# Kernel optimization log

Measured on AMD Instinct MI355X. Metric: run time of the kernel, lower is better.

Reference implementation:

```python
import jax, jax.numpy as jnp
import numpy as np

N = 100_000      # nodes
E = 1_600_000    # edges (before self-loops)
F_IN = 128       # num_features
H = 128          # nhid
G = 512          # graphs in batch
C = 10           # num_classes
EPS = 1e-5       # BatchNorm eps


def setup_inputs() -> dict:
    key = jax.random.key(0)
    ks = jax.random.split(key, 24)
    x = jax.random.normal(ks[0], (N, F_IN), jnp.float32)
    edge_index = jax.random.randint(ks[1], (2, E), 0, N, dtype=jnp.int64)
    batch = jnp.sort(jax.random.randint(ks[2], (N,), 0, G, dtype=jnp.int64))

    def lin(k, fi, fo):
        return jax.random.normal(k, (fi, fo), jnp.float32) / np.sqrt(fi).astype(np.float32)

    inp = dict(x=x, edge_index=edge_index, batch=batch)
    inp.update(
        W1=lin(ks[3], F_IN, H), b1=jnp.zeros((H,), jnp.float32),
        g1=jnp.ones((H,), jnp.float32), be1=jnp.zeros((H,), jnp.float32),
        W2=lin(ks[4], H, H), b2=jnp.zeros((H,), jnp.float32),
        g2=jnp.ones((H,), jnp.float32), be2=jnp.zeros((H,), jnp.float32),
        W3=lin(ks[5], H, H), b3=jnp.zeros((H,), jnp.float32),
        g3=jnp.ones((H,), jnp.float32), be3=jnp.zeros((H,), jnp.float32),
        gp=jnp.ones((H,), jnp.float32), bep=jnp.zeros((H,), jnp.float32),
        lw1=lin(ks[6], H, H), lb1=jnp.zeros((H,), jnp.float32),
        lw2=lin(ks[7], H, C), lb2=jnp.zeros((C,), jnp.float32),
    )
    return inp


def _batchnorm(h, g, b):
    # training-mode BatchNorm1d: batch stats, biased variance
    m = h.mean(axis=0)
    v = h.var(axis=0)
    return g * (h - m) * jax.lax.rsqrt(v + EPS) + b


def _gcn(h, W, b, src, dst, norm, n):
    # GCNConv: h @ W, then normalized gather-scatter aggregation
    h = h @ W
    msg = h[src] * norm[:, None]                     # [E+N, H] gather
    out = jax.ops.segment_sum(msg, dst, num_segments=n)
    return out + b


def reference(x, edge_index, batch, W1, b1, g1, be1, W2, b2, g2, be2,
              W3, b3, g3, be3, gp, bep, lw1, lb1, lw2, lb2):
    n = x.shape[0]
    loops = jnp.arange(n, dtype=edge_index.dtype)
    src = jnp.concatenate([edge_index[0], loops])
    dst = jnp.concatenate([edge_index[1], loops])
    # symmetric normalization D^{-1/2} (A+I) D^{-1/2}
    deg = jax.ops.segment_sum(jnp.ones_like(src, dtype=x.dtype), dst, num_segments=n)
    dis = jnp.where(deg > 0, jax.lax.rsqrt(jnp.maximum(deg, 1.0)), 0.0)
    norm = dis[src] * dis[dst]

    h = jax.nn.relu(_batchnorm(_gcn(x, W1, b1, src, dst, norm, n), g1, be1))
    h = jax.nn.relu(_batchnorm(_gcn(h, W2, b2, src, dst, norm, n), g2, be2))
    h = jax.nn.relu(_batchnorm(_gcn(h, W3, b3, src, dst, norm, n), g3, be3))

    # global_mean_pool over graph ids
    counts = jax.ops.segment_sum(jnp.ones((n,), x.dtype), batch, num_segments=G)
    pooled = jax.ops.segment_sum(h, batch, num_segments=G) / jnp.maximum(counts, 1.0)[:, None]

    z = _batchnorm(pooled, gp, bep)
    z = jax.nn.relu(z @ lw1 + lb1)
    # dropout_ratio=0.0 -> identity
    z = z @ lw2 + lb2
    return jax.nn.log_softmax(z, axis=-1)
```

## Files before the change

### kernel.cpp

```cpp
#include <hip/hip_runtime.h>
#include <hip/hip_bf16.h>
#include <cstdint>

#define HDIM 128

typedef __bf16 bf16x8 __attribute__((ext_vector_type(8)));
typedef unsigned short usx8 __attribute__((ext_vector_type(8)));
typedef float fx4 __attribute__((ext_vector_type(4)));

__device__ __forceinline__ float bf2f(unsigned short u) {
    unsigned int x = ((unsigned int)u) << 16;
    return __uint_as_float(x);
}
__device__ __forceinline__ unsigned short f2bf(float f) {
    unsigned int x = __float_as_uint(f);
    x += 0x7fffu + ((x >> 16) & 1u);
    return (unsigned short)(x >> 16);
}

__device__ __forceinline__ void detect_local(const unsigned int* xw, const unsigned int* eiw,
                                             int& f0, int& f1) {
    int sane = 0;
    for (int k = 0; k < 64; k++) {
        unsigned int w = xw[k];
        unsigned short ss[2] = {(unsigned short)(w & 0xffffu), (unsigned short)(w >> 16)};
        for (int q = 0; q < 2; q++) {
            int e = (ss[q] >> 7) & 0xFF;
            if ((ss[q] & 0x7fffu) == 0 || (e >= 100 && e <= 140)) sane++;
        }
    }
    f0 = (sane >= 110) ? 1 : 0;
    int zeros = 0;
    for (int k = 1; k < 64; k += 2)
        if (eiw[k] == 0) zeros++;
    f1 = (zeros >= 24) ? 1 : 0;
}

struct ParamTab {
    const void* p[15];
    int n[15];
    int off[15];
};

__global__ void phase1(const unsigned int* __restrict__ xw, const unsigned int* __restrict__ eiw,
                       const void* __restrict__ ei, const void* __restrict__ batch,
                       const void* __restrict__ W1, const void* __restrict__ W2,
                       const void* __restrict__ W3, ParamTab tab, int* __restrict__ flags,
                       float* __restrict__ gsumAll, int* __restrict__ Ct,
                       unsigned short* __restrict__ wconv, unsigned short* __restrict__ Wf,
                       int* __restrict__ goff, int* __restrict__ gcnt, int E, int N, int G,
                       int NB, int ntiles, int TILE) {
    __shared__ int h[1024];
    __shared__ int lf0s, lf1s;
    int b = blockIdx.x, t = threadIdx.x;
    if (t == 0) {
        int a0, a1;
        detect_local(xw, eiw, a0, a1);
        lf0s = a0;
        lf1s = a1;
    }
    __syncthreads();
    int lf0 = lf0s, lf1 = lf1s;
    if (b < ntiles) {
        for (int i = t; i < NB; i += 256) h[i] = 0;
        __syncthreads();
        int base = b * TILE;
        for (int i = t; i < TILE; i += 256) {
            int idx = base + i;
            if (idx < E) {
                int d = lf1 ? (int)((const long long*)ei)[(size_t)E + idx]
                            : ((const int*)ei)[(size_t)E + idx];
                atomicAdd(&h[d >> 9], 1);
            }
        }
        __syncthreads();
        for (int k = t; k < NB; k += 256) Ct[k * ntiles + b] = h[k];
    } else if (b < ntiles + 15) {
        int pb = b - ntiles;
        const void* src = tab.p[pb];
        int n = tab.n[pb];
        unsigned short* o = wconv + tab.off[pb];
        if (lf0) {
            const unsigned short* s = (const unsigned short*)src;
            for (int i = t; i < n; i += 256) o[i] = s[i];
        } else {
            const float* s = (const float*)src;
            for (int i = t; i < n; i += 256) o[i] = f2bf(s[i]);
        }
    } else if (b < ntiles + 17) {
        int gi = (b - ntiles - 15) * 256 + t;
        if (gi < G) {
            auto getb = [&](int i) -> int {
                return lf1 ? (int)((const long long*)batch)[i] : ((const int*)batch)[i];
            };
            auto lower = [&](int val) -> int {
                int lo = 0, hi = N;
                while (lo < hi) {
                    int mid = (lo + hi) >> 1;
                    if (getb(mid) < val) lo = mid + 1;
                    else hi = mid;
                }
                return lo;
            };
            int lo = lower(gi), hi = lower(gi + 1);
            goff[gi] = lo;
            gcnt[gi] = hi - lo;
        }
    } else if (b < ntiles + 17 + 24) {
        int idx = (b - ntiles - 17) * 256 + t;
        int layer = idx >> 11;
        int rem = idx & 2047;
        int kt = rem >> 9;
        int nt = (rem >> 6) & 7;
        int lane = rem & 63;
        const void* W = (layer == 0) ? W1 : ((layer == 1) ? W2 : W3);
        int row = lane & 15, quad = lane >> 4;
        unsigned short* o = Wf + ((size_t)layer * 2048 + (size_t)((kt * 8 + nt) * 64 + lane)) * 8;
#pragma unroll
        for (int j = 0; j < 8; j++) {
            int k = kt * 32 + quad * 8 + j;
            int off = k * HDIM + nt * 16 + row;
            o[j] = lf0 ? ((const unsigned short*)W)[off] : f2bf(((const float*)W)[off]);
        }
    } else {
        for (int i = t; i < 12288; i += 256) gsumAll[i] = 0.f;
        if (t == 0) {
            flags[0] = lf0;
            flags[1] = lf1;
        }
    }
}

__global__ void s1_scan(int* __restrict__ Ct, int* __restrict__ btot, int NB, int ntiles) {
    __shared__ int buf[512];
    int b = blockIdx.x, t = threadIdx.x;
    int v = (t < ntiles) ? Ct[b * ntiles + t] : 0;
    buf[t] = v;
    __syncthreads();
    for (int o = 1; o < 512; o <<= 1) {
        int a = (t >= o) ? buf[t - o] : 0;
        __syncthreads();
        buf[t] += a;
        __syncthreads();
    }
    if (t < ntiles) Ct[b * ntiles + t] = buf[t] - v;
    if (t == 0) btot[b] = buf[511];
}

__global__ void p1_scatter(const void* __restrict__ ei, const int* __restrict__ flags,
                           const int* __restrict__ Ct, const int* __restrict__ btot,
                           unsigned int* __restrict__ pairs, int E, int NB, int ntiles,
                           int TILE) {
    __shared__ int cur[1024];
    __shared__ int bb[256];
    int tile = blockIdx.x, t = threadIdx.x;
    int v = (t < NB) ? btot[t] : 0;
    bb[t] = v;
    __syncthreads();
    for (int o = 1; o < 256; o <<= 1) {
        int a = (t >= o) ? bb[t - o] : 0;
        __syncthreads();
        bb[t] += a;
        __syncthreads();
    }
    if (t < NB) cur[t] = (bb[t] - v) + Ct[t * ntiles + tile];
    __syncthreads();
    int base = tile * TILE;
    bool i64 = flags[1] != 0;
    for (int i = t; i < TILE; i += 256) {
        int idx = base + i;
        if (idx < E) {
            int s, d;
            if (i64) {
                s = (int)((const long long*)ei)[idx];
                d = (int)((const long long*)ei)[(size_t)E + idx];
            } else {
                s = ((const int*)ei)[idx];
                d = ((const int*)ei)[(size_t)E + idx];
            }
            int pos = atomicAdd(&cur[d >> 9], 1);
            pairs[pos] = ((unsigned)(d & 511) << 23) | (unsigned)s;
        }
    }
}

__global__ void p2_build(const unsigned int* __restrict__ pairs, const int* __restrict__ btot,
                         int* __restrict__ csrc, int* __restrict__ offs, int* __restrict__ cnt,
                         float* __restrict__ dis, int E, int N, int NB) {
    __shared__ int hist[512];
    __shared__ int start[512];
    __shared__ int cur[512];
    __shared__ int ps[256];
    __shared__ int bb[256];
    __shared__ int sh_excl[256];
    int b = blockIdx.x, t = threadIdx.x;
    int node0 = b * 512;
    int v = (t < NB) ? btot[t] : 0;
    bb[t] = v;
    __syncthreads();
    for (int o = 1; o < 256; o <<= 1) {
        int a = (t >= o) ? bb[t - o] : 0;
        __syncthreads();
        bb[t] += a;
        __syncthreads();
    }
    sh_excl[t] = bb[t] - v;
    for (int i = t; i < 512; i += 256) hist[i] = 0;
    __syncthreads();
    int lo = sh_excl[b];
    int hi = lo + ((b < NB) ? btot[b] : 0);
    for (int i = lo + t; i < hi; i += 256) {
        atomicAdd(&hist[pairs[i] >> 23], 1);
    }
    __syncthreads();
    ps[t] = hist[2 * t] + hist[2 * t + 1];
    __syncthreads();
    for (int o = 1; o < 256; o <<= 1) {
        int a = (t >= o) ? ps[t - o] : 0;
        __syncthreads();
        ps[t] += a;
        __syncthreads();
    }
    int e = t ? ps[t - 1] : 0;
    start[2 * t] = e;
    start[2 * t + 1] = e + hist[2 * t];
    __syncthreads();
    for (int i = t; i < 512; i += 256) {
        cur[i] = 0;
        int node = node0 + i;
        if (node < N) {
            offs[node] = lo + start[i];
            cnt[node] = hist[i];
            dis[node] = rsqrtf((float)(hist[i] + 1));
        }
    }
    __syncthreads();
    for (int i = lo + t; i < hi; i += 256) {
        unsigned int p = pairs[i];
        int l = p >> 23;
        int pos = lo + start[l] + atomicAdd(&cur[l], 1);
        csrc[pos] = (int)(p & 0x7fffffu);
    }
}

__global__ __launch_bounds__(256) void mm_mfma(const void* __restrict__ A,
                                               const unsigned short* __restrict__ Wf,
                                               unsigned short* __restrict__ C, int M,
                                               const float* __restrict__ gsumPrev,
                                               const unsigned short* __restrict__ gamma,
                                               const unsigned short* __restrict__ beta,
                                               const float* __restrict__ dis,
                                               const int* __restrict__ flags, int l0mode,
                                               float invn) {
    __shared__ float scs[128], shs[128];
    __shared__ unsigned short ldsC[4 * 16 * 136];
    int t = threadIdx.x;
    if (!l0mode && t < 128) {
        float s = 0.f, s2 = 0.f;
#pragma unroll
        for (int r = 0; r < 16; r++) {
            s += gsumPrev[r * 256 + t];
            s2 += gsumPrev[r * 256 + 128 + t];
        }
        float m = s * invn;
        float vv = s2 * invn - m * m;
        float sc = bf2f(gamma[t]) * rsqrtf(vv + 1e-5f);
        scs[t] = sc;
        shs[t] = bf2f(beta[t]) - m * sc;
    }
    __syncthreads();
    int gid = blockIdx.x * blockDim.x + t;
    int wave = gid >> 6;
    int lane = t & 63;
    int wv = t >> 6;
    int m0 = wave * 16;
    if (m0 >= M) return;
    int row = lane & 15, quad = lane >> 4;
    bool xfp32 = l0mode && !flags[0];
    const unsigned short* arow = (const unsigned short*)A + (size_t)(m0 + row) * HDIM + quad * 8;
    const float* arowf = (const float*)A + (size_t)(m0 + row) * HDIM + quad * 8;
    const unsigned short* ablk = (const unsigned short*)A;
    fx4 acc[8];
#pragma unroll
    for (int k = 0; k < 8; k++) acc[k] = (fx4){0.f, 0.f, 0.f, 0.f};
#pragma unroll
    for (int kt = 0; kt < 4; kt++) {
        bf16x8 a;
        if (xfp32) {
            fx4 f0 = *(const fx4*)(arowf + kt * 32);
            fx4 f1 = *(const fx4*)(arowf + kt * 32 + 4);
            usx8 tt;
#pragma unroll
            for (int q = 0; q < 4; q++) tt[q] = f2bf(f0[q]);
#pragma unroll
            for (int q = 0; q < 4; q++) tt[4 + q] = f2bf(f1[q]);
            a = __builtin_bit_cast(bf16x8, tt);
        } else if (l0mode) {
            usx8 raw = *(const usx8*)(arow + kt * 32);
            a = __builtin_bit_cast(bf16x8, raw);
        } else {
            int c0 = kt * 32 + quad * 8;
            usx8 raw =
                *(const usx8*)(ablk + ((size_t)(c0 >> 4) * M + (m0 + row)) * 16 + (c0 & 15));
            fx4 s0 = *(const fx4*)&scs[c0];
            fx4 s1 = *(const fx4*)&scs[c0 + 4];
            fx4 h0 = *(const fx4*)&shs[c0];
            fx4 h1 = *(const fx4*)&shs[c0 + 4];
            usx8 tt;
#pragma unroll
            for (int q = 0; q < 4; q++)
                tt[q] = f2bf(fmaxf(s0[q] * bf2f(raw[q]) + h0[q], 0.f));
#pragma unroll
            for (int q = 0; q < 4; q++)
                tt[4 + q] = f2bf(fmaxf(s1[q] * bf2f(raw[4 + q]) + h1[q], 0.f));
            a = __builtin_bit_cast(bf16x8, tt);
        }
        const unsigned short* wf = Wf + ((size_t)(kt * 8) * 64 + lane) * 8;
#pragma unroll
        for (int nt = 0; nt < 8; nt++) {
            bf16x8 bfr = __builtin_bit_cast(bf16x8, *(const usx8*)(wf + (size_t)nt * 64 * 8));
            acc[nt] = __builtin_amdgcn_mfma_f32_16x16x32_bf16(a, bfr, acc[nt], 0, 0, 0);
        }
    }
    float dsc[4];
#pragma unroll
    for (int r = 0; r < 4; r++) dsc[r] = dis[m0 + quad * 4 + r];
    unsigned short* lw = ldsC + wv * 16 * 136;
#pragma unroll
    for (int nt = 0; nt < 8; nt++) {
        int col = nt * 16 + row;
#pragma unroll
        for (int r = 0; r < 4; r++) {
            lw[(quad * 4 + r) * 136 + col] = f2bf(acc[nt][r] * dsc[r]);
        }
    }
    int sub8 = lane & 7, cbw = lane >> 3;
#pragma unroll
    for (int k = 0; k < 4; k++) {
        int ci = k * 8 + sub8;
        int nd = ci >> 1, half = ci & 1;
        if (m0 + nd < M) {
            const unsigned short* src = lw + nd * 136 + cbw * 16 + half * 8;
            unsigned short* dst = C + ((size_t)cbw * M + (m0 + nd)) * 16 + half * 8;
            *(usx8*)dst = *(const usx8*)src;
        }
    }
}

__global__ void aggregate(const unsigned short* __restrict__ hw, const float* __restrict__ dis,
                          const int* __restrict__ offs, const int* __restrict__ cnt,
                          const int* __restrict__ csrc, const unsigned short* __restrict__ bias,
                          unsigned short* __restrict__ agg, float* __restrict__ gsum16, int n) {
    __shared__ float red[256 * 8];
    int t = threadIdx.x;
    int lane = t & 63;
    int wv = t >> 6;
    int cb = blockIdx.x & 7;
    int gidx = blockIdx.x >> 3;
    int P = gridDim.x >> 3;
    int colOff = (lane & 1) * 8;
    usx8 bv = *(const usx8*)(bias + cb * 16 + colOff);
    const unsigned short* hslice = hw + (size_t)cb * n * 16;
    unsigned short* aslice = agg + (size_t)cb * n * 16;
    float csum[8], csq[8];
#pragma unroll
    for (int q = 0; q < 8; q++) {
        csum[q] = 0.f;
        csq[q] = 0.f;
    }
    for (int node0 = gidx * 128; node0 < n; node0 += P * 128) {
        int node = node0 + wv * 32 + (lane >> 1);
        if (node < n) {
            usx8 sv = *(const usx8*)(hslice + (size_t)node * 16 + colOff);
            float a[8];
#pragma unroll
            for (int q = 0; q < 8; q++) a[q] = bf2f(sv[q]);
            int o = offs[node], c = cnt[node];
            int s0 = (c > 0) ? csrc[o] : 0;
            int s1 = (c > 1) ? csrc[o + 1] : 0;
            int s2 = (c > 2) ? csrc[o + 2] : 0;
            int s3 = (c > 3) ? csrc[o + 3] : 0;
            int j = 0;
            while (j < c) {
                usx8 v0 = *(const usx8*)(hslice + (size_t)s0 * 16 + colOff);
                usx8 v1 = *(const usx8*)(hslice + (size_t)s1 * 16 + colOff);
                usx8 v2 = *(const usx8*)(hslice + (size_t)s2 * 16 + colOff);
                usx8 v3 = *(const usx8*)(hslice + (size_t)s3 * 16 + colOff);
                s0 = (j + 4 < c) ? csrc[o + j + 4] : 0;
                s1 = (j + 5 < c) ? csrc[o + j + 5] : 0;
                s2 = (j + 6 < c) ? csrc[o + j + 6] : 0;
                s3 = (j + 7 < c) ? csrc[o + j + 7] : 0;
#pragma unroll
                for (int q = 0; q < 8; q++) a[q] += bf2f(v0[q]);
                if (j + 1 < c) {
#pragma unroll
                    for (int q = 0; q < 8; q++) a[q] += bf2f(v1[q]);
                }
                if (j + 2 < c) {
#pragma unroll
                    for (int q = 0; q < 8; q++) a[q] += bf2f(v2[q]);
                }
                if (j + 3 < c) {
#pragma unroll
                    for (int q = 0; q < 8; q++) a[q] += bf2f(v3[q]);
                }
                j += 4;
            }
            float di = dis[node];
            usx8 ov;
#pragma unroll
            for (int q = 0; q < 8; q++) {
                float val = bf2f(bv[q]) + di * a[q];
                ov[q] = f2bf(val);
                float vr = bf2f(ov[q]);
                csum[q] += vr;
                csq[q] += vr * vr;
            }
            __builtin_nontemporal_store(ov, (usx8*)(aslice + (size_t)node * 16 + colOff));
        }
    }
    int rep = (gidx & 15) * 256;
#pragma unroll
    for (int q = 0; q < 8; q++) red[t * 8 + q] = csum[q];
    __syncthreads();
    for (int s = 128; s >= 2; s >>= 1) {
        if (t < s) {
#pragma unroll
            for (int q = 0; q < 8; q++) red[t * 8 + q] += red[(t + s) * 8 + q];
        }
        __syncthreads();
    }
    if (t < 2) {
#pragma unroll
        for (int q = 0; q < 8; q++)
            atomicAdd(&gsum16[rep + cb * 16 + t * 8 + q], red[t * 8 + q]);
    }
    __syncthreads();
#pragma unroll
    for (int q = 0; q < 8; q++) red[t * 8 + q] = csq[q];
    __syncthreads();
    for (int s = 128; s >= 2; s >>= 1) {
        if (t < s) {
#pragma unroll
            for (int q = 0; q < 8; q++) red[t * 8 + q] += red[(t + s) * 8 + q];
        }
        __syncthreads();
    }
    if (t < 2) {
#pragma unroll
        for (int q = 0; q < 8; q++)
            atomicAdd(&gsum16[rep + 128 + cb * 16 + t * 8 + q], red[t * 8 + q]);
    }
}

__global__ void pool(const unsigned short* __restrict__ hin, const int* __restrict__ goff,
                     const int* __restrict__ gcnt, const float* __restrict__ gsum3,
                     const unsigned short* __restrict__ gamma,
                     const unsigned short* __restrict__ beta, float* __restrict__ pooled,
                     float invn, int N_) {
    __shared__ float scs[128], shs[128];
    __shared__ float ls[256];
    int g = blockIdx.x, t = threadIdx.x;
    if (t < 128) {
        float s = 0.f, s2 = 0.f;
#pragma unroll
        for (int r = 0; r < 16; r++) {
            s += gsum3[r * 256 + t];
            s2 += gsum3[r * 256 + 128 + t];
        }
        float m = s * invn;
        float vv = s2 * invn - m * m;
        float sc = bf2f(gamma[t]) * rsqrtf(vv + 1e-5f);
        scs[t] = sc;
        shs[t] = bf2f(beta[t]) - m * sc;
    }
    __syncthreads();
    int c = t & 127, p = t >> 7;
    float scale = scs[c], shift = shs[c];
    int s = goff[g], cn = gcnt[g];
    const unsigned short* base = hin + (size_t)(c >> 4) * N_ * 16 + (c & 15);
    float acc = 0.f;
    for (int r = s + p; r < s + cn; r += 2)
        acc += fmaxf(scale * bf2f(base[(size_t)r * 16]) + shift, 0.f);
    ls[t] = acc;
    __syncthreads();
    if (t < 128) pooled[(size_t)g * HDIM + t] = (ls[t] + ls[t + 128]) / fmaxf((float)cn, 1.f);
}
__global__ void pooled_bn(const float* __restrict__ pooled, const unsigned short* __restrict__ g,
                          const unsigned short* __restrict__ be, float* __restrict__ psc,
                          float* __restrict__ psh, int G_) {
    int t = threadIdx.x;
    int c = t & 127, p = t >> 7;
    float s = 0.f, s2 = 0.f;
    for (int r = p; r < G_; r += 4) {
        float v = pooled[(size_t)r * HDIM + c];
        s += v;
        s2 += v * v;
    }
    __shared__ float ls[512], ls2[512];
    ls[t] = s;
    ls2[t] = s2;
    __syncthreads();
    if (t < 128) {
        float S = ls[t] + ls[t + 128] + ls[t + 256] + ls[t + 384];
        float S2 = ls2[t] + ls2[t + 128] + ls2[t + 256] + ls2[t + 384];
        float m = S / (float)G_;
        float v = S2 / (float)G_ - m * m;
        float sc = bf2f(g[t]) * rsqrtf(v + 1e-5f);
        psc[t] = sc;
        psh[t] = bf2f(be[t]) - m * sc;
    }
}
__global__ void mlp12(const float* __restrict__ pooled, const float* __restrict__ psc,
                      const float* __restrict__ psh, const unsigned short* __restrict__ lw1,
                      const unsigned short* __restrict__ lb1,
                      const unsigned short* __restrict__ lw2,
                      const unsigned short* __restrict__ lb2, void* __restrict__ out,
                      const int* __restrict__ flags) {
    int r = blockIdx.x, t = threadIdx.x;
    __shared__ float row[128];
    __shared__ float z1s[128];
    __shared__ float z2[10];
    __shared__ float lse;
    row[t] = psc[t] * pooled[(size_t)r * HDIM + t] + psh[t];
    __syncthreads();
    float acc = bf2f(lb1[t]);
    for (int k = 0; k < 128; k++) acc += row[k] * bf2f(lw1[k * HDIM + t]);
    z1s[t] = fmaxf(acc, 0.f);
    __syncthreads();
    if (t < 10) {
        float a = bf2f(lb2[t]);
        for (int k = 0; k < 128; k++) a += z1s[k] * bf2f(lw2[k * 10 + t]);
        z2[t] = a;
    }
    __syncthreads();
    if (t == 0) {
        float m = z2[0];
        for (int j = 1; j < 10; j++) m = fmaxf(m, z2[j]);
        float s = 0.f;
        for (int j = 0; j < 10; j++) s += expf(z2[j] - m);
        lse = m + logf(s);
    }
    __syncthreads();
    if (t < 10) {
        float v = z2[t] - lse;
        if (flags[0]) ((unsigned short*)out)[r * 10 + t] = f2bf(v);
        else ((float*)out)[r * 10 + t] = v;
    }
}

extern "C" void kernel_launch(void* const* d_in, const int* in_sizes, int n_in,
                              void* d_out, int out_size, void* d_ws, size_t ws_size,
                              hipStream_t stream) {
    const void* x = d_in[0];
    const void* ei = d_in[1];
    const void* batch = d_in[2];

    int N_ = in_sizes[2];
    int E_ = in_sizes[1] / 2;
    int G_ = out_size / 10;

    const int TILE = 4096;
    int NB = (N_ + 511) / 512;
    int ntiles = (E_ + TILE - 1) / TILE;
    int L = NB * ntiles;

    char* ws = (char*)d_ws;
    auto alloc = [&](size_t bytes) -> char* {
        char* p = ws;
        ws += (bytes + 255) & ~(size_t)255;
        return p;
    };
    int* flags = (int*)alloc(256);
    float* dis = (float*)alloc((size_t)N_ * 4);
    int* offs = (int*)alloc((size_t)N_ * 4);
    int* cnt = (int*)alloc((size_t)N_ * 4);
    int* Ct = (int*)alloc((size_t)L * 4);
    int* btot = (int*)alloc(1024);
    unsigned int* pairs = (unsigned int*)alloc((size_t)E_ * 4);
    int* csrc = (int*)alloc((size_t)E_ * 4);
    unsigned short* hw = (unsigned short*)alloc((size_t)N_ * HDIM * 2);
    unsigned short* aggbuf = (unsigned short*)alloc((size_t)N_ * HDIM * 2);
    unsigned short* wconv = (unsigned short*)alloc(70000 * 2);
    unsigned short* wfrag = (unsigned short*)alloc(3 * HDIM * HDIM * 2);
    float* gsumAll = (float*)alloc(12288 * 4);
    int* gcnt = (int*)alloc((size_t)G_ * 4);
    int* goff = (int*)alloc((size_t)G_ * 4);
    float* pooled = (float*)alloc((size_t)G_ * HDIM * 4);
    float* psc = (float*)alloc(128 * 4);
    float* psh = (float*)alloc(128 * 4);

    const int oB = 49152;
    const int oLB1 = oB + 1408;
    const int oLW1 = oLB1 + 128;
    const int oLW2 = oLW1 + 16384;
    const int oLB2 = oLW2 + 1280;

    ParamTab tab;
    const int srcIdx[15] = {4, 5, 6, 8, 9, 10, 12, 13, 14, 15, 16, 18, 17, 19, 20};
    const int dstOff[15] = {oB + 0, oB + 128, oB + 256,
                            oB + 384, oB + 512, oB + 640,
                            oB + 768, oB + 896, oB + 1024,
                            oB + 1152, oB + 1280,
                            oLB1, oLW1, oLW2, oLB2};
    for (int i = 0; i < 15; i++) {
        tab.p[i] = d_in[srcIdx[i]];
        tab.n[i] = in_sizes[srcIdx[i]];
        tab.off[i] = dstOff[i];
    }

    int p1_grid = ntiles + 15 + 2 + 24 + 1;
    phase1<<<p1_grid, 256, 0, stream>>>((const unsigned int*)x, (const unsigned int*)ei, ei,
                                        batch, d_in[3], d_in[7], d_in[11], tab, flags, gsumAll,
                                        Ct, wconv, wfrag, goff, gcnt, E_, N_, G_, NB, ntiles,
                                        TILE);
    s1_scan<<<NB, 512, 0, stream>>>(Ct, btot, NB, ntiles);
    p1_scatter<<<ntiles, 256, 0, stream>>>(ei, flags, Ct, btot, pairs, E_, NB, ntiles, TILE);
    p2_build<<<NB, 256, 0, stream>>>(pairs, btot, csrc, offs, cnt, dis, E_, N_, NB);

    int mm_blocks = (((N_ + 15) / 16) * 64 + 255) / 256;
    float invn = 1.f / (float)N_;

    for (int l = 0; l < 3; l++) {
        const void* A = (l == 0) ? x : (const void*)aggbuf;
        const float* gp = (l == 0) ? nullptr : (gsumAll + (size_t)(l - 1) * 4096);
        const unsigned short* gam = wconv + oB + (l ? (l - 1) * 384 + 128 : 0);
        const unsigned short* bet = wconv + oB + (l ? (l - 1) * 384 + 256 : 0);
        mm_mfma<<<mm_blocks, 256, 0, stream>>>(A, wfrag + (size_t)l * HDIM * HDIM, hw, N_, gp,
                                               gam, bet, dis, flags, (l == 0) ? 1 : 0, invn);
        aggregate<<<2048, 256, 0, stream>>>(hw, dis, offs, cnt, csrc, wconv + oB + l * 384,
                                            aggbuf, gsumAll + (size_t)l * 4096, N_);
    }

    pool<<<G_, 256, 0, stream>>>(aggbuf, goff, gcnt, gsumAll + 2 * 4096,
                                 wconv + oB + 2 * 384 + 128, wconv + oB + 2 * 384 + 256, pooled,
                                 invn, N_);
    pooled_bn<<<1, 512, 0, stream>>>(pooled, wconv + oB + 1152, wconv + oB + 1280, psc, psh, G_);
    mlp12<<<G_, 128, 0, stream>>>(pooled, psc, psh, wconv + oLW1, wconv + oLB1, wconv + oLW2,
                                  wconv + oLB2, d_out, flags);
}
```

Baseline: 604.1 us.

## Split each node's neighbor gather across 16 lanes with shared-memory index staging

The aggregate kernel now assigns 16 lanes per node, with 8 lane pairs each covering a strided subset of neighbors, and combines the partial sums with xor shuffles. Previously 2 lanes walked a node's whole neighbor list serially. Each block first stages its 128-node chunk of CSR source indices into shared memory (up to 8192 entries, falling back to global memory past that), and the shared buffer is reused for the final reduction. The goal is more memory-level parallelism and less per-thread imbalance on variable-degree nodes. In exchange it adds shuffle reductions, extra block barriers, and idle lanes on low-degree nodes.

```diff
diff --git a/kernel.cpp b/kernel.cpp
--- a/kernel.cpp
+++ b/kernel.cpp
@@ -347,79 +347,100 @@
     }
 }
 
-__global__ void aggregate(const unsigned short* __restrict__ hw, const float* __restrict__ dis,
-                          const int* __restrict__ offs, const int* __restrict__ cnt,
-                          const int* __restrict__ csrc, const unsigned short* __restrict__ bias,
-                          unsigned short* __restrict__ agg, float* __restrict__ gsum16, int n) {
-    __shared__ float red[256 * 8];
+__global__ __launch_bounds__(256) void aggregate(
+    const unsigned short* __restrict__ hw, const float* __restrict__ dis,
+    const int* __restrict__ offs, const int* __restrict__ cnt, const int* __restrict__ csrc,
+    const unsigned short* __restrict__ bias, unsigned short* __restrict__ agg,
+    float* __restrict__ gsum16, int n) {
+    __shared__ int sidx[8192];
     int t = threadIdx.x;
     int lane = t & 63;
     int wv = t >> 6;
+    int k = lane & 15;
+    int grpN = lane >> 4;
+    int pr = k >> 1;
+    int colOff = (k & 1) * 8;
     int cb = blockIdx.x & 7;
     int gidx = blockIdx.x >> 3;
     int P = gridDim.x >> 3;
-    int colOff = (lane & 1) * 8;
-    usx8 bv = *(const usx8*)(bias + cb * 16 + colOff);
     const unsigned short* hslice = hw + (size_t)cb * n * 16;
     unsigned short* aslice = agg + (size_t)cb * n * 16;
+    usx8 bv = *(const usx8*)(bias + cb * 16 + colOff);
     float csum[8], csq[8];
 #pragma unroll
     for (int q = 0; q < 8; q++) {
         csum[q] = 0.f;
         csq[q] = 0.f;
     }
-    for (int node0 = gidx * 128; node0 < n; node0 += P * 128) {
-        int node = node0 + wv * 32 + (lane >> 1);
-        if (node < n) {
-            usx8 sv = *(const usx8*)(hslice + (size_t)node * 16 + colOff);
-            float a[8];
-#pragma unroll
-            for (int q = 0; q < 8; q++) a[q] = bf2f(sv[q]);
-            int o = offs[node], c = cnt[node];
-            int s0 = (c > 0) ? csrc[o] : 0;
-            int s1 = (c > 1) ? csrc[o + 1] : 0;
-            int s2 = (c > 2) ? csrc[o + 2] : 0;
-            int s3 = (c > 3) ? csrc[o + 3] : 0;
-            int j = 0;
-            while (j < c) {
-                usx8 v0 = *(const usx8*)(hslice + (size_t)s0 * 16 + colOff);
-                usx8 v1 = *(const usx8*)(hslice + (size_t)s1 * 16 + colOff);
-                usx8 v2 = *(const usx8*)(hslice + (size_t)s2 * 16 + colOff);
-                usx8 v3 = *(const usx8*)(hslice + (size_t)s3 * 16 + colOff);
-                s0 = (j + 4 < c) ? csrc[o + j + 4] : 0;
-                s1 = (j + 5 < c) ? csrc[o + j + 5] : 0;
-                s2 = (j + 6 < c) ? csrc[o + j + 6] : 0;
-                s3 = (j + 7 < c) ? csrc[o + j + 7] : 0;
-#pragma unroll
-                for (int q = 0; q < 8; q++) a[q] += bf2f(v0[q]);
-                if (j + 1 < c) {
-#pragma unroll
-                    for (int q = 0; q < 8; q++) a[q] += bf2f(v1[q]);
+    for (int chunk = gidx * 128; chunk < n; chunk += P * 128) {
+        int last = (chunk + 127 < n) ? (chunk + 127) : (n - 1);
+        int base = offs[chunk];
+        int cend = offs[last] + cnt[last];
+        int len = cend - base;
+        if (len > 8192) len = 8192;
+        __syncthreads();
+        for (int i = t; i < len; i += 256) sidx[i] = csrc[base + i];
+        __syncthreads();
+        for (int sr = 0; sr < 8; sr++) {
+            int node = chunk + wv * 32 + sr * 4 + grpN;
+            if (node < n) {
+                int o = offs[node], c = cnt[node];
+                float a[8];
+#pragma unroll
+                for (int q = 0; q < 8; q++) a[q] = 0.f;
+                auto ldidx = [&](int pos) -> int {
+                    int r = pos - base;
+                    return (r < 8192) ? sidx[r] : csrc[pos];
+                };
+                int jA = pr, jB = pr + 8;
+                bool vA = jA < c, vB = jB < c;
+                int sA = vA ? ldidx(o + jA) : 0;
+                int sB = vB ? ldidx(o + jB) : 0;
+                for (int j = 0; j < c; j += 16) {
+                    bool cA = vA, cB = vB;
+                    int tA = sA, tB = sB;
+                    int nA = j + 16 + pr, nB = j + 24 + pr;
+                    vA = nA < c;
+                    vB = nB < c;
+                    sA = vA ? ldidx(o + nA) : 0;
+                    sB = vB ? ldidx(o + nB) : 0;
+                    usx8 va = *(const usx8*)(hslice + (size_t)tA * 16 + colOff);
+                    usx8 vb = *(const usx8*)(hslice + (size_t)tB * 16 + colOff);
+                    if (cA) {
+#pragma unroll
+                        for (int q = 0; q < 8; q++) a[q] += bf2f(va[q]);
+                    }
+                    if (cB) {
+#pragma unroll
+                        for (int q = 0; q < 8; q++) a[q] += bf2f(vb[q]);
+                    }
                 }
-                if (j + 2 < c) {
-#pragma unroll
-                    for (int q = 0; q < 8; q++) a[q] += bf2f(v2[q]);
+#pragma unroll
+                for (int d = 2; d <= 8; d <<= 1) {
+#pragma unroll
+                    for (int q = 0; q < 8; q++) a[q] += __shfl_xor(a[q], d, 64);
                 }
-                if (j + 3 < c) {
-#pragma unroll
-                    for (int q = 0; q < 8; q++) a[q] += bf2f(v3[q]);
+                if (k < 2) {
+                    usx8 sv = *(const usx8*)(hslice + (size_t)node * 16 + colOff);
+                    float di = dis[node];
+                    usx8 ov;
+#pragma unroll
+                    for (int q = 0; q < 8; q++) {
+                        float val = bf2f(bv[q]) + di * (a[q] + bf2f(sv[q]));
+                        ov[q] = f2bf(val);
+                        float vr = bf2f(ov[q]);
+                        csum[q] += vr;
+                        csq[q] += vr * vr;
+                    }
+                    __builtin_nontemporal_store(ov,
+                                                (usx8*)(aslice + (size_t)node * 16 + colOff));
                 }
-                j += 4;
             }
-            float di = dis[node];
-            usx8 ov;
-#pragma unroll
-            for (int q = 0; q < 8; q++) {
-                float val = bf2f(bv[q]) + di * a[q];
-                ov[q] = f2bf(val);
-                float vr = bf2f(ov[q]);
-                csum[q] += vr;
-                csq[q] += vr * vr;
-            }
-            __builtin_nontemporal_store(ov, (usx8*)(aslice + (size_t)node * 16 + colOff));
-        }
-    }
+        }
+    }
+    float* red = (float*)sidx;
     int rep = (gidx & 15) * 256;
+    __syncthreads();
 #pragma unroll
     for (int q = 0; q < 8; q++) red[t * 8 + q] = csum[q];
     __syncthreads();
```

Result: slower. 700.0 us (+15.9%).
